# Kernel optimization log

Measured on AMD Instinct MI355X. Metric: run time of the kernel, lower is better.

Reference implementation:

```python
import jax, jax.numpy as jnp
import numpy as np

B, H, S, D = 4, 16, 2048, 64
TEMPERATURE = 8.0  # sqrt(D)
NEG = -1000000000.0

def setup_inputs() -> dict:
    key = jax.random.key(0)
    kq, kk, kv, km = jax.random.split(key, 4)
    q = jax.random.normal(kq, (B, H, S, D), dtype=jnp.float32)
    k = jax.random.normal(kk, (B, H, S, D), dtype=jnp.float32)
    v = jax.random.normal(kv, (B, H, S, D), dtype=jnp.float32)
    mask = jax.random.randint(km, (B, 1, S, S), 0, 2, dtype=jnp.int32)
    return {"q": q, "k": k, "v": v, "mask": mask}

def reference(q, k, v, mask):
    # scores: [B,H,S,S]
    scores = jnp.einsum('bhqd,bhkd->bhqk', q / TEMPERATURE, k)
    scores = jnp.where(mask == 1, NEG, scores)
    attn = jax.nn.softmax(scores, axis=-1)  # dropout p=0.0 -> identity
    out = jnp.einsum('bhqk,bhkd->bhqd', attn, v)
    return out
```

## Files before the change

kernel.cpp:

```cpp
#include <hip/hip_runtime.h>

#define NB 4
#define NH 16
#define SS 2048
#define DD 64
#define QT 256
#define KT 64
#define NT (SS / KT)
#define KSP 72
#define QSCALE 0.18033688011112042f

#define WS_BITS_BYTES ((size_t)NB * SS * (SS / 8))
#define WS_KB_OFF  ((size_t)2  << 20)
#define WS_VB_OFF  ((size_t)18 << 20)
#define WS_FULL    ((size_t)34 << 20)

typedef __bf16 bf16x8 __attribute__((ext_vector_type(8)));
typedef __bf16 bf16x2 __attribute__((ext_vector_type(2)));
typedef float  floatx16 __attribute__((ext_vector_type(16)));
typedef unsigned long long u64t;

static_assert(sizeof(bf16x8) == 16, "bf16x8 must be 16B");

__device__ __forceinline__ int pack2(float a, float b) {
    bf16x2 v; v[0] = (__bf16)a; v[1] = (__bf16)b;
    return __builtin_bit_cast(int, v);
}

__device__ __forceinline__ int vperm_inv(int c) {
    return 16 * ((c >> 4) & 3) + 8 * ((c >> 2) & 1) + 4 * ((c >> 3) & 1) + (c & 3);
}

__global__ __launch_bounds__(256)
void pack_mask_kernel(const int* __restrict__ M, u64t* __restrict__ bits)
{
    const int w    = (blockIdx.x * 256 + threadIdx.x) >> 6;
    const int lane = threadIdx.x & 63;
    #pragma unroll 4
    for (int i = 0; i < 16; ++i) {
        const int gw   = i * 16384 + w;
        const size_t row = (size_t)(gw >> 5);
        const int word = gw & 31;
        const int mval = M[row * SS + (size_t)word * 64 + lane];
        const u64t b = __ballot(mval == 1);
        if (lane == 0) bits[gw] = b;
    }
}

__global__ __launch_bounds__(256)
void pre_kernel(const float* __restrict__ K, const float* __restrict__ V,
                const int* __restrict__ M, u64t* __restrict__ bits,
                __bf16* __restrict__ KB, __bf16* __restrict__ VB)
{
    __shared__ float vt[64][68];
    const int t = threadIdx.x;

    if (blockIdx.x < 2048) {
        const int bh = blockIdx.x >> 5;
        const int tt = blockIdx.x & 31;
        const size_t tb = (size_t)bh * SS * DD + (size_t)tt * (KT * DD);

        {
            const float* src = K + tb + t * 16;
            __bf16* dst = KB + tb + t * 16;
            float4 f0 = ((const float4*)src)[0];
            float4 f1 = ((const float4*)src)[1];
            float4 f2 = ((const float4*)src)[2];
            float4 f3 = ((const float4*)src)[3];
            bf16x8 o0, o1;
            o0[0]=(__bf16)f0.x; o0[1]=(__bf16)f0.y; o0[2]=(__bf16)f0.z; o0[3]=(__bf16)f0.w;
            o0[4]=(__bf16)f1.x; o0[5]=(__bf16)f1.y; o0[6]=(__bf16)f1.z; o0[7]=(__bf16)f1.w;
            o1[0]=(__bf16)f2.x; o1[1]=(__bf16)f2.y; o1[2]=(__bf16)f2.z; o1[3]=(__bf16)f2.w;
            o1[4]=(__bf16)f3.x; o1[5]=(__bf16)f3.y; o1[6]=(__bf16)f3.z; o1[7]=(__bf16)f3.w;
            ((bf16x8*)dst)[0] = o0;
            ((bf16x8*)dst)[1] = o1;
        }

        {
            const int key = t >> 2, ds = (t & 3) * 16;
            const float* src = V + tb + (size_t)key * DD + ds;
            #pragma unroll
            for (int i = 0; i < 4; ++i)
                *(float4*)&vt[key][ds + 4 * i] = ((const float4*)src)[i];
        }
        __syncthreads();
        {
            const int dim = t >> 2, cb = (t & 3) * 16;
            bf16x8 o0, o1;
            #pragma unroll
            for (int c = 0; c < 16; ++c) {
                const float vvv = vt[vperm_inv(cb + c)][dim];
                if (c < 8) o0[c] = (__bf16)vvv; else o1[c - 8] = (__bf16)vvv;
            }
            __bf16* dst = VB + tb + (size_t)dim * 64 + cb;
            ((bf16x8*)dst)[0] = o0;
            ((bf16x8*)dst)[1] = o1;
        }
    } else {
        const int w    = ((blockIdx.x - 2048) * 256 + t) >> 6;
        const int lane = t & 63;
        #pragma unroll 4
        for (int i = 0; i < 16; ++i) {
            const int gw   = i * 16384 + w;
            const size_t row = (size_t)(gw >> 5);
            const int word = gw & 31;
            const int mval = M[row * SS + (size_t)word * 64 + lane];
            const u64t b = __ballot(mval == 1);
            if (lane == 0) bits[gw] = b;
        }
    }
}

template<int MODE>
__global__ __launch_bounds__(512, 4)
void attn_kernel(const float* __restrict__ Q, const float* __restrict__ K,
                 const float* __restrict__ V, const int* __restrict__ M,
                 const unsigned* __restrict__ MB,
                 const __bf16* __restrict__ KB, const __bf16* __restrict__ VB,
                 float* __restrict__ O)
{
    __shared__ __bf16 ks [2][KT][KSP];
    __shared__ __bf16 vsT[2][DD][KSP];

    const int t    = threadIdx.x;
    const int wave = t >> 6;
    const int lane = t & 63;
    const int l31  = lane & 31;
    const int h8   = lane >> 5;

    const int bh    = blockIdx.x & 63;
    const int qtile = blockIdx.x >> 6;
    const int b     = bh >> 4;
    const int q0    = qtile * QT + wave * 32;

    const size_t base = (size_t)bh * SS * DD;

    bf16x8 aq[4];
    {
        const float* qp = Q + base + (size_t)(q0 + l31) * DD + 8 * h8;
        #pragma unroll
        for (int s = 0; s < 4; ++s) {
            float4 f0 = *(const float4*)(qp + 16 * s);
            float4 f1 = *(const float4*)(qp + 16 * s + 4);
            bf16x8 a;
            a[0] = (__bf16)(f0.x * QSCALE); a[1] = (__bf16)(f0.y * QSCALE);
            a[2] = (__bf16)(f0.z * QSCALE); a[3] = (__bf16)(f0.w * QSCALE);
            a[4] = (__bf16)(f1.x * QSCALE); a[5] = (__bf16)(f1.y * QSCALE);
            a[6] = (__bf16)(f1.z * QSCALE); a[7] = (__bf16)(f1.w * QSCALE);
            aq[s] = a;
        }
    }

    bf16x8 ones8;
    #pragma unroll
    for (int i = 0; i < 8; ++i) ones8[i] = (__bf16)1.0f;

    const int srow = t >> 3;
    const int sc8  = (t & 7) * 8;
    const __bf16* kbp = KB + base + (size_t)srow * DD + sc8;
    const __bf16* vbp = VB + base + (size_t)srow * DD + sc8;
    bf16x8 kreg, vreg;

    const int skey = t >> 3;
    const int sdc  = (t & 7) * 8;
    const int vk   = 2 * (t & 31);
    const int vdc  = (t >> 5) * 4;
    const int vcol = 16 * (vk >> 4) + 8 * ((vk >> 2) & 1) + (vk & 3) + 4 * ((vk >> 3) & 1);
    const float* kp0 = K + base + (size_t)skey * DD + sdc;
    const float* vp0 = V + base + (size_t)vk * DD + vdc;
    float4 ka0, ka1, va0, va1;

    if constexpr (MODE == 2) {
        kreg = *(const bf16x8*)kbp;
        vreg = *(const bf16x8*)vbp;
    } else {
        ka0 = ((const float4*)kp0)[0];
        ka1 = ((const float4*)kp0)[1];
        va0 = *(const float4*)(vp0);
        va1 = *(const float4*)(vp0 + DD);
    }

    const u64t* mbrow = (const u64t*)MB + ((size_t)b * SS + q0 + l31) * (SS / 64);
    const int*  mrow  = M + (size_t)b * SS * SS + (size_t)(q0 + l31) * SS + 4 * h8;
    u64t mall = 0, mnext = 0;
    if constexpr (MODE >= 1) mall = mbrow[0];

    floatx16 o0, o1, oL;
    #pragma unroll
    for (int i = 0; i < 16; ++i) { o0[i] = 0.f; o1[i] = 0.f; oL[i] = 0.f; }

    for (int tt = 0; tt < NT; ++tt) {
        const int cur = tt & 1;

        if constexpr (MODE == 2) {
            *(bf16x8*)&ks [cur][srow][sc8] = kreg;
            *(bf16x8*)&vsT[cur][srow][sc8] = vreg;
        } else {
            bf16x8 kw;
            kw[0]=(__bf16)ka0.x; kw[1]=(__bf16)ka0.y; kw[2]=(__bf16)ka0.z; kw[3]=(__bf16)ka0.w;
            kw[4]=(__bf16)ka1.x; kw[5]=(__bf16)ka1.y; kw[6]=(__bf16)ka1.z; kw[7]=(__bf16)ka1.w;
            *(bf16x8*)&ks[cur][skey][sdc] = kw;
            #pragma unroll
            for (int i = 0; i < 4; ++i) {
                bf16x2 pr;
                pr[0] = (__bf16)(&va0.x)[i]; pr[1] = (__bf16)(&va1.x)[i];
                *(bf16x2*)&vsT[cur][vdc + i][vcol] = pr;
            }
        }
        __syncthreads();

        int4 mi[8];
        if constexpr (MODE == 0) {
            #pragma unroll
            for (int g = 0; g < 8; ++g)
                mi[g] = *(const int4*)(mrow + tt * KT + 8 * g);
        }

        if constexpr (MODE == 2) {
            const size_t jn = (size_t)((tt + 1) & (NT - 1)) * (KT * DD);
            kreg = *(const bf16x8*)(kbp + jn);
            vreg = *(const bf16x8*)(vbp + jn);
        } else {
            const int jn = ((tt + 1) * KT) & (SS - 1);
            const float* kn = kp0 + (size_t)jn * DD;
            ka0 = ((const float4*)kn)[0];
            ka1 = ((const float4*)kn)[1];
            const float* vn = vp0 + (size_t)jn * DD;
            va0 = *(const float4*)(vn);
            va1 = *(const float4*)(vn + DD);
        }
        if constexpr (MODE >= 1) mnext = mbrow[(tt + 1) & (NT - 1)];

        #pragma unroll
        for (int half = 0; half < 2; ++half) {
            floatx16 c;
            if constexpr (MODE >= 1) {
                const unsigned u = (unsigned)(mall >> (32 * half)) >> (4 * h8);
                #pragma unroll
                for (int i = 0; i < 16; ++i) {
                    const int pos = (i & 3) + 8 * (i >> 2);
                    const int sm = ((int)(u << (31 - pos))) >> 31;
                    c[i] = __builtin_bit_cast(float, sm & (int)0xC4800000u);
                }
            } else {
                #pragma unroll
                for (int i = 0; i < 16; ++i) {
                    const int g2 = 4 * half + (i >> 2);
                    c[i] = ((&mi[g2].x)[i & 3] == 1) ? -1024.0f : 0.0f;
                }
            }

            __builtin_amdgcn_s_setprio(1);
            #pragma unroll
            for (int s = 0; s < 4; ++s) {
                bf16x8 a = *(const bf16x8*)&ks[cur][32 * half + l31][16 * s + 8 * h8];
                c = __builtin_amdgcn_mfma_f32_32x32x16_bf16(a, aq[s], c, 0, 0, 0);
            }
            __builtin_amdgcn_s_setprio(0);

            int pk[8];
            #pragma unroll
            for (int g = 0; g < 8; ++g) {
                float pa = __builtin_amdgcn_exp2f(c[2 * g]);
                float pb = __builtin_amdgcn_exp2f(c[2 * g + 1]);
                pk[g] = pack2(pa, pb);
            }

            __builtin_amdgcn_s_setprio(1);
            #pragma unroll
            for (int s2 = 0; s2 < 2; ++s2) {
                int4 fw; fw.x = pk[4*s2]; fw.y = pk[4*s2+1]; fw.z = pk[4*s2+2]; fw.w = pk[4*s2+3];
                bf16x8 bp = __builtin_bit_cast(bf16x8, fw);
                bf16x8 av0 = *(const bf16x8*)&vsT[cur][l31]     [32 * half + 16 * s2 + 8 * h8];
                bf16x8 av1 = *(const bf16x8*)&vsT[cur][32 + l31][32 * half + 16 * s2 + 8 * h8];
                o0 = __builtin_amdgcn_mfma_f32_32x32x16_bf16(av0, bp, o0, 0, 0, 0);
                o1 = __builtin_amdgcn_mfma_f32_32x32x16_bf16(av1, bp, o1, 0, 0, 0);
                oL = __builtin_amdgcn_mfma_f32_32x32x16_bf16(ones8, bp, oL, 0, 0, 0);
            }
            __builtin_amdgcn_s_setprio(0);
        }

        if constexpr (MODE >= 1) mall = mnext;
    }

    float inv = 1.0f / oL[0];
    float* op = O + base + (size_t)(q0 + l31) * DD;
    #pragma unroll
    for (int s = 0; s < 4; ++s) {
        float4 st0, st1;
        st0.x = o0[4*s+0] * inv; st0.y = o0[4*s+1] * inv;
        st0.z = o0[4*s+2] * inv; st0.w = o0[4*s+3] * inv;
        st1.x = o1[4*s+0] * inv; st1.y = o1[4*s+1] * inv;
        st1.z = o1[4*s+2] * inv; st1.w = o1[4*s+3] * inv;
        *(float4*)(op + 8 * s + 4 * h8)      = st0;
        *(float4*)(op + 32 + 8 * s + 4 * h8) = st1;
    }
}

extern "C" void kernel_launch(void* const* d_in, const int* in_sizes, int n_in,
                              void* d_out, int out_size, void* d_ws, size_t ws_size,
                              hipStream_t stream) {
    (void)in_sizes; (void)n_in; (void)out_size;
    const float* q = (const float*)d_in[0];
    const float* k = (const float*)d_in[1];
    const float* v = (const float*)d_in[2];
    const int*   m = (const int*)d_in[3];
    float* out = (float*)d_out;
    dim3 grid(NB * NH * (SS / QT));

    if (ws_size >= WS_FULL) {
        u64t*   bits = (u64t*)d_ws;
        __bf16* kb16 = (__bf16*)((char*)d_ws + WS_KB_OFF);
        __bf16* vb16 = (__bf16*)((char*)d_ws + WS_VB_OFF);
        pre_kernel<<<dim3(6144), 256, 0, stream>>>(k, v, m, bits, kb16, vb16);
        attn_kernel<2><<<grid, 512, 0, stream>>>(q, k, v, m, (const unsigned*)bits,
                                                 kb16, vb16, out);
    } else if (ws_size >= WS_BITS_BYTES) {
        u64t* bits = (u64t*)d_ws;
        pack_mask_kernel<<<dim3(4096), 256, 0, stream>>>(m, bits);
        attn_kernel<1><<<grid, 512, 0, stream>>>(q, k, v, m, (const unsigned*)bits,
                                                 nullptr, nullptr, out);
    } else {
        attn_kernel<0><<<grid, 512, 0, stream>>>(q, k, v, m, nullptr,
                                                 nullptr, nullptr, out);
    }
}
```

Baseline: 272.1 us.

## Prepack V in MFMA fragment order and load it straight to registers

The V preprocessing kernel now writes bf16 V in per-lane MFMA fragment order, so in MODE 2 each wave loads its V operands directly from global memory into registers and skips the shared-memory staging and its LDS reads. The V shared buffer shrinks to a single unused copy in MODE 2, and the barrier becomes a raw s_barrier that waits only on LDS counters. In exchange, every wave in a block re-reads the same V tile from global/L2 (8x redundancy across waves), and the loads issued right before use may expose latency.

Result: slower. 339.2 us (+24.7%).

```diff
diff --git a/kernel.cpp b/kernel.cpp
--- a/kernel.cpp
+++ b/kernel.cpp
@@ -27,6 +27,9 @@
     return __builtin_bit_cast(int, v);
 }
 
+__device__ __forceinline__ int vperm_col(int k) {
+    return 16 * (k >> 4) + 8 * ((k >> 2) & 1) + (k & 3) + 4 * ((k >> 3) & 1);
+}
 __device__ __forceinline__ int vperm_inv(int c) {
     return 16 * ((c >> 4) & 3) + 8 * ((c >> 2) & 1) + 4 * ((c >> 3) & 1) + (c & 3);
 }
@@ -84,17 +87,21 @@
                 *(float4*)&vt[key][ds + 4 * i] = ((const float4*)src)[i];
         }
         __syncthreads();
+
         {
-            const int dim = t >> 2, cb = (t & 3) * 16;
-            bf16x8 o0, o1;
-            #pragma unroll
-            for (int c = 0; c < 16; ++c) {
-                const float vvv = vt[vperm_inv(cb + c)][dim];
-                if (c < 8) o0[c] = (__bf16)vvv; else o1[c - 8] = (__bf16)vvv;
-            }
-            __bf16* dst = VB + tb + (size_t)dim * 64 + cb;
-            ((bf16x8*)dst)[0] = o0;
-            ((bf16x8*)dst)[1] = o1;
+            #pragma unroll
+            for (int rep = 0; rep < 2; ++rep) {
+                const int sIdx = t + 256 * rep;
+                const int g = sIdx >> 6, l = sIdx & 63;
+                const int half = g >> 2, s2 = (g >> 1) & 1, a = g & 1;
+                const int colb = 32 * half + 16 * s2 + 8 * (l >> 5);
+                const int dim  = 32 * a + (l & 31);
+                bf16x8 o;
+                #pragma unroll
+                for (int j = 0; j < 8; ++j)
+                    o[j] = (__bf16)vt[vperm_inv(colb + j)][dim];
+                *(bf16x8*)(VB + tb + (size_t)sIdx * 8) = o;
+            }
         }
     } else {
         const int w    = ((blockIdx.x - 2048) * 256 + t) >> 6;
@@ -120,7 +127,7 @@
                  float* __restrict__ O)
 {
     __shared__ __bf16 ks [2][KT][KSP];
-    __shared__ __bf16 vsT[2][DD][KSP];
+    __shared__ __bf16 vsT[(MODE == 2) ? 1 : 2][DD][KSP];
 
     const int t    = threadIdx.x;
     const int wave = t >> 6;
@@ -158,21 +165,22 @@
     const int srow = t >> 3;
     const int sc8  = (t & 7) * 8;
     const __bf16* kbp = KB + base + (size_t)srow * DD + sc8;
-    const __bf16* vbp = VB + base + (size_t)srow * DD + sc8;
-    bf16x8 kreg, vreg;
+    bf16x8 kreg;
+
+    const __bf16* vfp = VB + base + (size_t)lane * 8;
+    bf16x8 vfr[8];
 
     const int skey = t >> 3;
     const int sdc  = (t & 7) * 8;
     const int vk   = 2 * (t & 31);
     const int vdc  = (t >> 5) * 4;
-    const int vcol = 16 * (vk >> 4) + 8 * ((vk >> 2) & 1) + (vk & 3) + 4 * ((vk >> 3) & 1);
+    const int vcol = vperm_col(vk);
     const float* kp0 = K + base + (size_t)skey * DD + sdc;
     const float* vp0 = V + base + (size_t)vk * DD + vdc;
     float4 ka0, ka1, va0, va1;
 
     if constexpr (MODE == 2) {
         kreg = *(const bf16x8*)kbp;
-        vreg = *(const bf16x8*)vbp;
     } else {
         ka0 = ((const float4*)kp0)[0];
         ka1 = ((const float4*)kp0)[1];
@@ -193,8 +201,11 @@
         const int cur = tt & 1;
 
         if constexpr (MODE == 2) {
-            *(bf16x8*)&ks [cur][srow][sc8] = kreg;
-            *(bf16x8*)&vsT[cur][srow][sc8] = vreg;
+            *(bf16x8*)&ks[cur][srow][sc8] = kreg;
+            const __bf16* vt0 = vfp + (size_t)tt * (8 * 512);
+            #pragma unroll
+            for (int g = 0; g < 8; ++g)
+                vfr[g] = *(const bf16x8*)(vt0 + g * 512);
         } else {
             bf16x8 kw;
             kw[0]=(__bf16)ka0.x; kw[1]=(__bf16)ka0.y; kw[2]=(__bf16)ka0.z; kw[3]=(__bf16)ka0.w;
@@ -207,7 +218,14 @@
                 *(bf16x2*)&vsT[cur][vdc + i][vcol] = pr;
             }
         }
-        __syncthreads();
+
+        if constexpr (MODE == 2) {
+            asm volatile("s_waitcnt lgkmcnt(0)" ::: "memory");
+            __builtin_amdgcn_s_barrier();
+            asm volatile("" ::: "memory");
+        } else {
+            __syncthreads();
+        }
 
         int4 mi[8];
         if constexpr (MODE == 0) {
@@ -219,7 +237,6 @@
         if constexpr (MODE == 2) {
             const size_t jn = (size_t)((tt + 1) & (NT - 1)) * (KT * DD);
             kreg = *(const bf16x8*)(kbp + jn);
-            vreg = *(const bf16x8*)(vbp + jn);
         } else {
             const int jn = ((tt + 1) * KT) & (SS - 1);
             const float* kn = kp0 + (size_t)jn * DD;
@@ -271,8 +288,14 @@
             for (int s2 = 0; s2 < 2; ++s2) {
                 int4 fw; fw.x = pk[4*s2]; fw.y = pk[4*s2+1]; fw.z = pk[4*s2+2]; fw.w = pk[4*s2+3];
                 bf16x8 bp = __builtin_bit_cast(bf16x8, fw);
-                bf16x8 av0 = *(const bf16x8*)&vsT[cur][l31]     [32 * half + 16 * s2 + 8 * h8];
-                bf16x8 av1 = *(const bf16x8*)&vsT[cur][32 + l31][32 * half + 16 * s2 + 8 * h8];
+                bf16x8 av0, av1;
+                if constexpr (MODE == 2) {
+                    av0 = vfr[half * 4 + s2 * 2 + 0];
+                    av1 = vfr[half * 4 + s2 * 2 + 1];
+                } else {
+                    av0 = *(const bf16x8*)&vsT[cur][l31]     [32 * half + 16 * s2 + 8 * h8];
+                    av1 = *(const bf16x8*)&vsT[cur][32 + l31][32 * half + 16 * s2 + 8 * h8];
+                }
                 o0 = __builtin_amdgcn_mfma_f32_32x32x16_bf16(av0, bp, o0, 0, 0, 0);
                 o1 = __builtin_amdgcn_mfma_f32_32x32x16_bf16(av1, bp, o1, 0, 0, 0);
                 oL = __builtin_amdgcn_mfma_f32_32x32x16_bf16(ones8, bp, oL, 0, 0, 0);
```

## Add 4-wave attention kernel with 64 query rows per wave for bf16 path

Applied to the files above, without the earlier changes.

Adds a dedicated kernel for the precomputed bf16 K/V path where each wave handles two 32-row query groups sharing each K/V LDS fragment read. Blocks shrink from 512 to 256 threads, and each thread loads two K/V rows per tile. The goal is to halve LDS reads per MFMA and reduce block-level barrier cost, using a raw s_barrier with an explicit lgkmcnt wait. The cost is roughly double the accumulator and register pressure per wave, which may lower occupancy.

Measured after the change: 271.4 us. No clear change (-0.3%).

```diff
diff --git a/kernel.cpp b/kernel.cpp
--- a/kernel.cpp
+++ b/kernel.cpp
@@ -27,6 +27,9 @@
     return __builtin_bit_cast(int, v);
 }
 
+__device__ __forceinline__ int vperm_col(int k) {
+    return 16 * (k >> 4) + 8 * ((k >> 2) & 1) + (k & 3) + 4 * ((k >> 3) & 1);
+}
 __device__ __forceinline__ int vperm_inv(int c) {
     return 16 * ((c >> 4) & 3) + 8 * ((c >> 2) & 1) + 4 * ((c >> 3) & 1) + (c & 3);
 }
@@ -111,13 +114,177 @@
     }
 }
 
+__global__ __launch_bounds__(256, 2)
+void attn2_kernel(const float* __restrict__ Q, const unsigned* __restrict__ MBu,
+                  const __bf16* __restrict__ KB, const __bf16* __restrict__ VB,
+                  float* __restrict__ O)
+{
+    __shared__ __bf16 ks [2][KT][KSP];
+    __shared__ __bf16 vsT[2][DD][KSP];
+
+    const int t    = threadIdx.x;
+    const int wave = t >> 6;
+    const int lane = t & 63;
+    const int l31  = lane & 31;
+    const int h8   = lane >> 5;
+
+    const int bh    = blockIdx.x & 63;
+    const int qtile = blockIdx.x >> 6;
+    const int b     = bh >> 4;
+    const int q0    = qtile * QT + wave * 64;
+
+    const size_t base = (size_t)bh * SS * DD;
+
+    bf16x8 aqA[4], aqB[4];
+    #pragma unroll
+    for (int grp = 0; grp < 2; ++grp) {
+        const float* qp = Q + base + (size_t)(q0 + 32 * grp + l31) * DD + 8 * h8;
+        #pragma unroll
+        for (int s = 0; s < 4; ++s) {
+            float4 f0 = *(const float4*)(qp + 16 * s);
+            float4 f1 = *(const float4*)(qp + 16 * s + 4);
+            bf16x8 a;
+            a[0] = (__bf16)(f0.x * QSCALE); a[1] = (__bf16)(f0.y * QSCALE);
+            a[2] = (__bf16)(f0.z * QSCALE); a[3] = (__bf16)(f0.w * QSCALE);
+            a[4] = (__bf16)(f1.x * QSCALE); a[5] = (__bf16)(f1.y * QSCALE);
+            a[6] = (__bf16)(f1.z * QSCALE); a[7] = (__bf16)(f1.w * QSCALE);
+            if (grp == 0) aqA[s] = a; else aqB[s] = a;
+        }
+    }
+
+    bf16x8 ones8;
+    #pragma unroll
+    for (int i = 0; i < 8; ++i) ones8[i] = (__bf16)1.0f;
+
+    const int srow = t >> 3;
+    const int sc8  = (t & 7) * 8;
+    const __bf16* kbp = KB + base + (size_t)srow * DD + sc8;
+    const __bf16* vbp = VB + base + (size_t)srow * DD + sc8;
+    bf16x8 kr0, kr1, vr0, vr1;
+
+    kr0 = *(const bf16x8*)kbp;
+    kr1 = *(const bf16x8*)(kbp + 32 * DD);
+    vr0 = *(const bf16x8*)vbp;
+    vr1 = *(const bf16x8*)(vbp + 32 * DD);
+
+    const u64t* mbrA = (const u64t*)MBu + ((size_t)b * SS + q0 + l31)      * (SS / 64);
+    const u64t* mbrB = (const u64t*)MBu + ((size_t)b * SS + q0 + 32 + l31) * (SS / 64);
+    u64t mA = mbrA[0], mB = mbrB[0], mnA, mnB;
+
+    floatx16 o0A, o1A, oLA, o0B, o1B, oLB;
+    #pragma unroll
+    for (int i = 0; i < 16; ++i) {
+        o0A[i] = 0.f; o1A[i] = 0.f; oLA[i] = 0.f;
+        o0B[i] = 0.f; o1B[i] = 0.f; oLB[i] = 0.f;
+    }
+
+    for (int tt = 0; tt < NT; ++tt) {
+        const int cur = tt & 1;
+
+        *(bf16x8*)&ks [cur][srow]     [sc8] = kr0;
+        *(bf16x8*)&ks [cur][srow + 32][sc8] = kr1;
+        *(bf16x8*)&vsT[cur][srow]     [sc8] = vr0;
+        *(bf16x8*)&vsT[cur][srow + 32][sc8] = vr1;
+
+        asm volatile("s_waitcnt lgkmcnt(0)" ::: "memory");
+        __builtin_amdgcn_s_barrier();
+        asm volatile("" ::: "memory");
+
+        {
+            const size_t jn = (size_t)((tt + 1) & (NT - 1)) * (KT * DD);
+            kr0 = *(const bf16x8*)(kbp + jn);
+            kr1 = *(const bf16x8*)(kbp + jn + 32 * DD);
+            vr0 = *(const bf16x8*)(vbp + jn);
+            vr1 = *(const bf16x8*)(vbp + jn + 32 * DD);
+        }
+        mnA = mbrA[(tt + 1) & (NT - 1)];
+        mnB = mbrB[(tt + 1) & (NT - 1)];
+
+        #pragma unroll
+        for (int half = 0; half < 2; ++half) {
+            floatx16 cA, cB;
+            {
+                const unsigned uA = (unsigned)(mA >> (32 * half)) >> (4 * h8);
+                const unsigned uB = (unsigned)(mB >> (32 * half)) >> (4 * h8);
+                #pragma unroll
+                for (int i = 0; i < 16; ++i) {
+                    const int pos = (i & 3) + 8 * (i >> 2);
+                    const int sA = ((int)(uA << (31 - pos))) >> 31;
+                    const int sB = ((int)(uB << (31 - pos))) >> 31;
+                    cA[i] = __builtin_bit_cast(float, sA & (int)0xC4800000u);
+                    cB[i] = __builtin_bit_cast(float, sB & (int)0xC4800000u);
+                }
+            }
+
+            __builtin_amdgcn_s_setprio(1);
+            #pragma unroll
+            for (int s = 0; s < 4; ++s) {
+                bf16x8 a = *(const bf16x8*)&ks[cur][32 * half + l31][16 * s + 8 * h8];
+                cA = __builtin_amdgcn_mfma_f32_32x32x16_bf16(a, aqA[s], cA, 0, 0, 0);
+                cB = __builtin_amdgcn_mfma_f32_32x32x16_bf16(a, aqB[s], cB, 0, 0, 0);
+            }
+            __builtin_amdgcn_s_setprio(0);
+
+            int pkA[8], pkB[8];
+            #pragma unroll
+            for (int g = 0; g < 8; ++g) {
+                float a0 = __builtin_amdgcn_exp2f(cA[2 * g]);
+                float a1 = __builtin_amdgcn_exp2f(cA[2 * g + 1]);
+                float b0 = __builtin_amdgcn_exp2f(cB[2 * g]);
+                float b1 = __builtin_amdgcn_exp2f(cB[2 * g + 1]);
+                pkA[g] = pack2(a0, a1);
+                pkB[g] = pack2(b0, b1);
+            }
+
+            __builtin_amdgcn_s_setprio(1);
+            #pragma unroll
+            for (int s2 = 0; s2 < 2; ++s2) {
+                bf16x8 av0 = *(const bf16x8*)&vsT[cur][l31]     [32 * half + 16 * s2 + 8 * h8];
+                bf16x8 av1 = *(const bf16x8*)&vsT[cur][32 + l31][32 * half + 16 * s2 + 8 * h8];
+                int4 fwA; fwA.x = pkA[4*s2]; fwA.y = pkA[4*s2+1]; fwA.z = pkA[4*s2+2]; fwA.w = pkA[4*s2+3];
+                int4 fwB; fwB.x = pkB[4*s2]; fwB.y = pkB[4*s2+1]; fwB.z = pkB[4*s2+2]; fwB.w = pkB[4*s2+3];
+                bf16x8 bpA = __builtin_bit_cast(bf16x8, fwA);
+                bf16x8 bpB = __builtin_bit_cast(bf16x8, fwB);
+                o0A = __builtin_amdgcn_mfma_f32_32x32x16_bf16(av0, bpA, o0A, 0, 0, 0);
+                o0B = __builtin_amdgcn_mfma_f32_32x32x16_bf16(av0, bpB, o0B, 0, 0, 0);
+                o1A = __builtin_amdgcn_mfma_f32_32x32x16_bf16(av1, bpA, o1A, 0, 0, 0);
+                o1B = __builtin_amdgcn_mfma_f32_32x32x16_bf16(av1, bpB, o1B, 0, 0, 0);
+                oLA = __builtin_amdgcn_mfma_f32_32x32x16_bf16(ones8, bpA, oLA, 0, 0, 0);
+                oLB = __builtin_amdgcn_mfma_f32_32x32x16_bf16(ones8, bpB, oLB, 0, 0, 0);
+            }
+            __builtin_amdgcn_s_setprio(0);
+        }
+
+        mA = mnA; mB = mnB;
+    }
+
+    const float invA = 1.0f / oLA[0];
+    const float invB = 1.0f / oLB[0];
+    float* opA = O + base + (size_t)(q0 + l31) * DD;
+    float* opB = O + base + (size_t)(q0 + 32 + l31) * DD;
+    #pragma unroll
+    for (int s = 0; s < 4; ++s) {
+        float4 st;
+        st.x = o0A[4*s+0] * invA; st.y = o0A[4*s+1] * invA;
+        st.z = o0A[4*s+2] * invA; st.w = o0A[4*s+3] * invA;
+        *(float4*)(opA + 8 * s + 4 * h8) = st;
+        st.x = o1A[4*s+0] * invA; st.y = o1A[4*s+1] * invA;
+        st.z = o1A[4*s+2] * invA; st.w = o1A[4*s+3] * invA;
+        *(float4*)(opA + 32 + 8 * s + 4 * h8) = st;
+        st.x = o0B[4*s+0] * invB; st.y = o0B[4*s+1] * invB;
+        st.z = o0B[4*s+2] * invB; st.w = o0B[4*s+3] * invB;
+        *(float4*)(opB + 8 * s + 4 * h8) = st;
+        st.x = o1B[4*s+0] * invB; st.y = o1B[4*s+1] * invB;
+        st.z = o1B[4*s+2] * invB; st.w = o1B[4*s+3] * invB;
+        *(float4*)(opB + 32 + 8 * s + 4 * h8) = st;
+    }
+}
+
 template<int MODE>
 __global__ __launch_bounds__(512, 4)
 void attn_kernel(const float* __restrict__ Q, const float* __restrict__ K,
                  const float* __restrict__ V, const int* __restrict__ M,
-                 const unsigned* __restrict__ MB,
-                 const __bf16* __restrict__ KB, const __bf16* __restrict__ VB,
-                 float* __restrict__ O)
+                 const unsigned* __restrict__ MB, float* __restrict__ O)
 {
     __shared__ __bf16 ks [2][KT][KSP];
     __shared__ __bf16 vsT[2][DD][KSP];
@@ -155,30 +322,18 @@
     #pragma unroll
     for (int i = 0; i < 8; ++i) ones8[i] = (__bf16)1.0f;
 
-    const int srow = t >> 3;
-    const int sc8  = (t & 7) * 8;
-    const __bf16* kbp = KB + base + (size_t)srow * DD + sc8;
-    const __bf16* vbp = VB + base + (size_t)srow * DD + sc8;
-    bf16x8 kreg, vreg;
-
     const int skey = t >> 3;
     const int sdc  = (t & 7) * 8;
     const int vk   = 2 * (t & 31);
     const int vdc  = (t >> 5) * 4;
-    const int vcol = 16 * (vk >> 4) + 8 * ((vk >> 2) & 1) + (vk & 3) + 4 * ((vk >> 3) & 1);
+    const int vcol = vperm_col(vk);
     const float* kp0 = K + base + (size_t)skey * DD + sdc;
     const float* vp0 = V + base + (size_t)vk * DD + vdc;
-    float4 ka0, ka1, va0, va1;
-
-    if constexpr (MODE == 2) {
-        kreg = *(const bf16x8*)kbp;
-        vreg = *(const bf16x8*)vbp;
-    } else {
-        ka0 = ((const float4*)kp0)[0];
-        ka1 = ((const float4*)kp0)[1];
-        va0 = *(const float4*)(vp0);
-        va1 = *(const float4*)(vp0 + DD);
-    }
+
+    float4 ka0 = ((const float4*)kp0)[0];
+    float4 ka1 = ((const float4*)kp0)[1];
+    float4 va0 = *(const float4*)(vp0);
+    float4 va1 = *(const float4*)(vp0 + DD);
 
     const u64t* mbrow = (const u64t*)MB + ((size_t)b * SS + q0 + l31) * (SS / 64);
     const int*  mrow  = M + (size_t)b * SS * SS + (size_t)(q0 + l31) * SS + 4 * h8;
@@ -192,10 +347,7 @@
     for (int tt = 0; tt < NT; ++tt) {
         const int cur = tt & 1;
 
-        if constexpr (MODE == 2) {
-            *(bf16x8*)&ks [cur][srow][sc8] = kreg;
-            *(bf16x8*)&vsT[cur][srow][sc8] = vreg;
-        } else {
+        {
             bf16x8 kw;
             kw[0]=(__bf16)ka0.x; kw[1]=(__bf16)ka0.y; kw[2]=(__bf16)ka0.z; kw[3]=(__bf16)ka0.w;
             kw[4]=(__bf16)ka1.x; kw[5]=(__bf16)ka1.y; kw[6]=(__bf16)ka1.z; kw[7]=(__bf16)ka1.w;
@@ -216,11 +368,7 @@
                 mi[g] = *(const int4*)(mrow + tt * KT + 8 * g);
         }
 
-        if constexpr (MODE == 2) {
-            const size_t jn = (size_t)((tt + 1) & (NT - 1)) * (KT * DD);
-            kreg = *(const bf16x8*)(kbp + jn);
-            vreg = *(const bf16x8*)(vbp + jn);
-        } else {
+        {
             const int jn = ((tt + 1) * KT) & (SS - 1);
             const float* kn = kp0 + (size_t)jn * DD;
             ka0 = ((const float4*)kn)[0];
@@ -313,15 +461,13 @@
         __bf16* kb16 = (__bf16*)((char*)d_ws + WS_KB_OFF);
         __bf16* vb16 = (__bf16*)((char*)d_ws + WS_VB_OFF);
         pre_kernel<<<dim3(6144), 256, 0, stream>>>(k, v, m, bits, kb16, vb16);
-        attn_kernel<2><<<grid, 512, 0, stream>>>(q, k, v, m, (const unsigned*)bits,
-                                                 kb16, vb16, out);
+        attn2_kernel<<<grid, 256, 0, stream>>>(q, (const unsigned*)bits,
+                                               kb16, vb16, out);
     } else if (ws_size >= WS_BITS_BYTES) {
         u64t* bits = (u64t*)d_ws;
         pack_mask_kernel<<<dim3(4096), 256, 0, stream>>>(m, bits);
-        attn_kernel<1><<<grid, 512, 0, stream>>>(q, k, v, m, (const unsigned*)bits,
-                                                 nullptr, nullptr, out);
+        attn_kernel<1><<<grid, 512, 0, stream>>>(q, k, v, m, (const unsigned*)bits, out);
     } else {
-        attn_kernel<0><<<grid, 512, 0, stream>>>(q, k, v, m, nullptr,
-                                                 nullptr, nullptr, out);
-    }
-}
+        attn_kernel<0><<<grid, 512, 0, stream>>>(q, k, v, m, nullptr, out);
+    }
+}
```
